# Optimization experiments

Measured on AMD Instinct MI355X. Metric: run time of the kernel, lower is better.

Reference implementation:

```python
import jax, jax.numpy as jnp
import numpy as np

NEG_SLOPE = 0.2


def gat_layer(x, W, a_src, a_dst, b, src, dst, num_nodes, heads, out_c, concat):
    # Linear transform per head: [N, heads, out_c]
    h = (x @ W).reshape(num_nodes, heads, out_c)
    # Per-node attention logits for source/dest roles: [N, heads]
    e_src = jnp.einsum('nhc,hc->nh', h, a_src)
    e_dst = jnp.einsum('nhc,hc->nh', h, a_dst)
    # Edge-wise scores (gather), LeakyReLU: [E, heads]
    e = jax.nn.leaky_relu(e_src[src] + e_dst[dst], negative_slope=NEG_SLOPE)
    # Segment softmax over incoming edges of each destination node
    m = jax.ops.segment_max(e, dst, num_segments=num_nodes)
    ex = jnp.exp(e - m[dst])
    denom = jax.ops.segment_sum(ex, dst, num_segments=num_nodes)
    alpha = ex / denom[dst]                       # [E, heads]
    # Weighted scatter-aggregate of source messages: [N, heads, out_c]
    out = jax.ops.segment_sum(h[src] * alpha[:, :, None], dst, num_segments=num_nodes)
    if concat:
        out = out.reshape(num_nodes, heads * out_c)
    else:
        out = out.mean(axis=1)
    return out + b


def setup_inputs() -> dict:
    key = jax.random.key(0)
    ks = jax.random.split(key, 12)
    N, E = 50000, 800000
    in_c, out_c, heads = 128, 32, 4
    x = jax.random.normal(ks[0], (N, in_c), dtype=jnp.float32)
    edge_index = jax.random.randint(ks[1], (2, E), 0, N, dtype=jnp.int64)
    s1 = 1.0 / np.sqrt(in_c)
    W1 = jax.random.normal(ks[2], (in_c, heads * out_c), dtype=jnp.float32) * s1
    a_src1 = jax.random.normal(ks[3], (heads, out_c), dtype=jnp.float32) * 0.1
    a_dst1 = jax.random.normal(ks[4], (heads, out_c), dtype=jnp.float32) * 0.1
    b1 = jnp.zeros((heads * out_c,), dtype=jnp.float32)
    s2 = 1.0 / np.sqrt(heads * out_c)
    W2 = jax.random.normal(ks[5], (heads * out_c, out_c), dtype=jnp.float32) * s2
    a_src2 = jax.random.normal(ks[6], (1, out_c), dtype=jnp.float32) * 0.1
    a_dst2 = jax.random.normal(ks[7], (1, out_c), dtype=jnp.float32) * 0.1
    b2 = jnp.zeros((out_c,), dtype=jnp.float32)
    return {"x": x, "edge_index": edge_index, "W1": W1, "a_src1": a_src1,
            "a_dst1": a_dst1, "b1": b1, "W2": W2, "a_src2": a_src2,
            "a_dst2": a_dst2, "b2": b2}


def reference(x, edge_index, W1, a_src1, a_dst1, b1, W2, a_src2, a_dst2, b2):
    N = x.shape[0]
    heads, out_c = a_src1.shape
    # add_self_loops=True (PyG default)
    loops = jnp.arange(N, dtype=edge_index.dtype)
    src = jnp.concatenate([edge_index[0], loops])
    dst = jnp.concatenate([edge_index[1], loops])
    h1 = gat_layer(x, W1, a_src1, a_dst1, b1, src, dst, N, heads, out_c, concat=True)
    h1 = jax.nn.elu(h1)
    out = gat_layer(h1, W2, a_src2, a_dst2, b2, src, dst, N, 1, out_c, concat=False)
    return out
```

## Files before the change

### kernel.cpp

```cpp
#include <hip/hip_runtime.h>
#include <hip/hip_bf16.h>

#define LRELU_SLOPE 0.2f
#define NB_SHIFT 7
#define NBLK 512

typedef __attribute__((ext_vector_type(8))) short short8;
typedef __attribute__((ext_vector_type(4))) float float4v;

__device__ inline float b2f(unsigned short u) {
    union { unsigned int i; float f; } v; v.i = ((unsigned int)u) << 16; return v.f;
}
__device__ inline unsigned short f2b(float f) {
    union { float f; unsigned int i; } v; v.f = f;
    unsigned int x = v.i;
    unsigned int r = x + 0x7fffu + ((x >> 16) & 1u);
    return (unsigned short)(r >> 16);
}
__device__ inline float lrelu(float x) { return x > 0.f ? x : LRELU_SLOPE * x; }

__global__ __launch_bounds__(256) void gemm1_mfma_kernel(
        const float* __restrict__ x, const float* __restrict__ W1,
        const float* __restrict__ a_src, const float* __restrict__ a_dst,
        unsigned short* __restrict__ h1b, float* __restrict__ es,
        float* __restrict__ ed, int N,
        const int* __restrict__ dst, int E, int Etot, int nb, int chunk,
        int* __restrict__ cnt) {
    __shared__ unsigned short xs[64][136];
    __shared__ unsigned short wt[128][136];
    int tid = threadIdx.x;
    int n0 = blockIdx.x * 64;

    for (int i = tid; i < 128 * 128; i += 256) {
        int k = i >> 7, n = i & 127;
        wt[n][k] = f2b(W1[i]);
    }
    {
        int rows = N - n0; if (rows > 64) rows = 64;
        const float4* xv = (const float4*)(x + (size_t)n0 * 128);
        int lim = rows * 32;
        for (int i = tid; i < lim; i += 256) {
            float4 v = xv[i];
            int r = i >> 5, c4 = (i & 31) << 2;
            uint2 p;
            p.x = (unsigned int)f2b(v.x) | ((unsigned int)f2b(v.y) << 16);
            p.y = (unsigned int)f2b(v.z) | ((unsigned int)f2b(v.w) << 16);
            *(uint2*)&xs[r][c4] = p;
        }
    }
    __syncthreads();

    int wave = tid >> 6;
    int lane = tid & 63;
    int lrow = lane & 15;
    int quad = lane >> 4;

    short8 afr[4];
#pragma unroll
    for (int kc = 0; kc < 4; kc++)
        afr[kc] = *(const short8*)&xs[wave * 16 + lrow][kc * 32 + quad * 8];
    __syncthreads();

#pragma unroll
    for (int ct = 0; ct < 8; ct++) {
        float4v acc = {0.f, 0.f, 0.f, 0.f};
#pragma unroll
        for (int kc = 0; kc < 4; kc++) {
            short8 bfr = *(const short8*)&wt[ct * 16 + lrow][kc * 32 + quad * 8];
            acc = __builtin_amdgcn_mfma_f32_16x16x32_bf16(afr[kc], bfr, acc, 0, 0, 0);
        }
#pragma unroll
        for (int r = 0; r < 4; r++) {
            int lr = wave * 16 + quad * 4 + r;
            int grow = n0 + lr;
            unsigned short hb = f2b(acc[r]);
            xs[lr][ct * 16 + lrow] = hb;
            if (grow < N)
                h1b[grow * 128 + ct * 16 + lrow] = hb;
        }
    }
    __syncthreads();

    int row = tid >> 2, h = tid & 3;
    int rg = n0 + row;
    if (rg < N) {
        const float* ap = a_src + h * 32;
        const float* bp = a_dst + h * 32;
        float s = 0.f, d = 0.f;
#pragma unroll
        for (int c2 = 0; c2 < 16; c2++) {
            unsigned int u = *(const unsigned int*)&xs[row][h * 32 + 2 * c2];
            float v0 = b2f((unsigned short)(u & 0xffffu));
            float v1 = b2f((unsigned short)(u >> 16));
            float2 a = *(const float2*)&ap[2 * c2];
            float2 b = *(const float2*)&bp[2 * c2];
            s += v0 * a.x + v1 * a.y;
            d += v0 * b.x + v1 * b.y;
        }
        es[rg * 4 + h] = s;
        ed[rg * 4 + h] = d;
    }

    int* histm = (int*)&wt[0][0];
    int blk = blockIdx.x;
    if (blk < NBLK)
        for (int i = tid; i < nb; i += 256) histm[i] = 0;
    __syncthreads();
    if (blk < NBLK) {
        int lo = blk * chunk;
        int hi = lo + chunk; if (hi > Etot) hi = Etot;
        for (int i = lo + tid; i < hi; i += 256) {
            int d = (i < E) ? dst[i] : (i - E);
            atomicAdd(&histm[d >> NB_SHIFT], 1);
        }
    }
    __syncthreads();
    if (blk < NBLK)
        for (int b = tid; b < nb; b += 256)
            cnt[b * NBLK + blk] = histm[b];
}

__global__ __launch_bounds__(1024) void scanA_kernel(int* cnt, int* bsum, int M) {
    __shared__ int tile[1024];
    int i = blockIdx.x * 1024 + threadIdx.x;
    int v = (i < M) ? cnt[i] : 0;
    tile[threadIdx.x] = v;
    __syncthreads();
    for (int off = 1; off < 1024; off <<= 1) {
        int t = (threadIdx.x >= (unsigned)off) ? tile[threadIdx.x - off] : 0;
        __syncthreads();
        tile[threadIdx.x] += t;
        __syncthreads();
    }
    int incl = tile[threadIdx.x];
    if (i < M) cnt[i] = incl - v;
    if (threadIdx.x == 1023) bsum[blockIdx.x] = incl;
}

__device__ inline void boff_scan(const int* __restrict__ bsum, int nbA,
                                 int* boffl, int tid) {
    int v = (tid < nbA) ? bsum[tid] : 0;
    boffl[tid] = v;
    __syncthreads();
    for (int off = 1; off < 256; off <<= 1) {
        int t = (tid >= off) ? boffl[tid - off] : 0;
        __syncthreads();
        boffl[tid] += t;
        __syncthreads();
    }
    int excl = boffl[tid] - v;
    __syncthreads();
    boffl[tid] = excl;
    __syncthreads();
}

__global__ __launch_bounds__(256) void partition_kernel(
        const int* __restrict__ src, const int* __restrict__ dst,
        int E, int Etot, int nb, int chunk, int nbA,
        const int* __restrict__ cnt, const int* __restrict__ bsum,
        unsigned int* __restrict__ bkt) {
    __shared__ int cur[512];
    __shared__ int boffl[256];
    int tid = threadIdx.x;
    boff_scan(bsum, nbA, boffl, tid);
    int blk = blockIdx.x;
    for (int b = tid; b < nb; b += 256) {
        int idx = b * NBLK + blk;
        cur[b] = cnt[idx] + boffl[idx >> 10];
    }
    __syncthreads();
    int lo = blk * chunk;
    int hi = lo + chunk; if (hi > Etot) hi = Etot;
    for (int i = lo + tid; i < hi; i += 256) {
        int s, d;
        if (i < E) { s = src[i]; d = dst[i]; }
        else       { s = d = i - E; }
        int pos = atomicAdd(&cur[d >> NB_SHIFT], 1);
        bkt[pos] = ((unsigned int)(d & 127) << 20) | (unsigned int)s;
    }
}

__global__ __launch_bounds__(256) void finalize_kernel(
        const unsigned int* __restrict__ bkt, const int* __restrict__ cnt,
        const int* __restrict__ bsum, int nb, int nbA,
        const float* __restrict__ es, const float* __restrict__ ed,
        int* __restrict__ ptr, int* __restrict__ csr_src,
        _Float16* __restrict__ w1h, int N, int Etot) {
    __shared__ int deg[128];
    __shared__ int scn[128];
    __shared__ int cur[128];
    __shared__ int boffl[256];
    int tid = threadIdx.x;
    boff_scan(bsum, nbA, boffl, tid);
    int b = blockIdx.x;
    int idx0 = b * NBLK;
    int base = cnt[idx0] + boffl[idx0 >> 10];
    int nextbase;
    if (b + 1 < nb) {
        int idx1 = (b + 1) * NBLK;
        nextbase = cnt[idx1] + boffl[idx1 >> 10];
    } else nextbase = Etot;
    int count = nextbase - base;
    int node0 = b << NB_SHIFT;
    int nodes = N - node0; if (nodes > 128) nodes = 128;

    if (tid < 128) deg[tid] = 0;
    __syncthreads();
    for (int i = tid; i < count; i += 256)
        atomicAdd(&deg[bkt[base + i] >> 20], 1);
    __syncthreads();
    int v = (tid < 128) ? deg[tid] : 0;
    if (tid < 128) scn[tid] = v;
    __syncthreads();
    for (int off = 1; off < 128; off <<= 1) {
        int t = (tid < 128 && tid >= (unsigned)off) ? scn[tid - off] : 0;
        __syncthreads();
        if (tid < 128) scn[tid] += t;
        __syncthreads();
    }
    if (tid < 128) {
        int excl = scn[tid] - v;
        cur[tid] = excl;
        if (tid < nodes) ptr[node0 + tid] = base + excl;
    }
    if (b == nb - 1 && tid == 0) ptr[N] = Etot;
    __syncthreads();
    for (int i = tid; i < count; i += 256) {
        unsigned int p = bkt[base + i];
        int dloc = p >> 20;
        int s = (int)(p & 0xFFFFFu);
        int pos = base + atomicAdd(&cur[dloc], 1);
        csr_src[pos] = s;
        float4 a = *(const float4*)&es[s * 4];
        float4 bb = *(const float4*)&ed[(node0 + dloc) * 4];
        union { _Float16 h[4]; uint2 u; } ww;
        ww.h[0] = (_Float16)__expf(lrelu(a.x + bb.x));
        ww.h[1] = (_Float16)__expf(lrelu(a.y + bb.y));
        ww.h[2] = (_Float16)__expf(lrelu(a.z + bb.z));
        ww.h[3] = (_Float16)__expf(lrelu(a.w + bb.w));
        *(uint2*)&w1h[(size_t)pos * 4] = ww.u;
    }
}

__global__ __launch_bounds__(256) void gemm2_mfma_kernel(
        const unsigned short* __restrict__ h1e, const float* __restrict__ W2,
        const float* __restrict__ a_src, const float* __restrict__ a_dst,
        unsigned short* __restrict__ h2b, float* __restrict__ es,
        float* __restrict__ ed, int N) {
    __shared__ unsigned short xs[64][136];
    __shared__ unsigned short wt[32][136];
    int tid = threadIdx.x;
    int n0 = blockIdx.x * 64;

    for (int i = tid; i < 128 * 32; i += 256) {
        int k = i >> 5, n = i & 31;
        wt[n][k] = f2b(W2[i]);
    }
    {
        const unsigned int* srcp = (const unsigned int*)(h1e + (size_t)n0 * 128);
        int rows = (N - n0) < 64 ? (N - n0) : 64;
        int maxu = rows * 64;
        for (int i = tid; i < 4096; i += 256) {
            unsigned int v = (i < maxu) ? srcp[i] : 0u;
            int r = i >> 6, cp = (i & 63) << 1;
            *(unsigned int*)&xs[r][cp] = v;
        }
    }
    __syncthreads();

    int wave = tid >> 6;
    int lane = tid & 63;
    int lrow = lane & 15;
    int quad = lane >> 4;

    short8 afr[4];
#pragma unroll
    for (int kc = 0; kc < 4; kc++)
        afr[kc] = *(const short8*)&xs[wave * 16 + lrow][kc * 32 + quad * 8];
    __syncthreads();

#pragma unroll
    for (int ct = 0; ct < 2; ct++) {
        float4v acc = {0.f, 0.f, 0.f, 0.f};
#pragma unroll
        for (int kc = 0; kc < 4; kc++) {
            short8 bfr = *(const short8*)&wt[ct * 16 + lrow][kc * 32 + quad * 8];
            acc = __builtin_amdgcn_mfma_f32_16x16x32_bf16(afr[kc], bfr, acc, 0, 0, 0);
        }
#pragma unroll
        for (int r = 0; r < 4; r++) {
            int lr = wave * 16 + quad * 4 + r;
            int grow = n0 + lr;
            unsigned short hb = f2b(acc[r]);
            xs[lr][ct * 16 + lrow] = hb;
            if (grow < N)
                h2b[(size_t)grow * 32 + ct * 16 + lrow] = hb;
        }
    }
    __syncthreads();

    if (tid < 64) {
        int rg = n0 + tid;
        if (rg < N) {
            float s = 0.f, d = 0.f;
#pragma unroll
            for (int c2 = 0; c2 < 16; c2++) {
                unsigned int u = *(const unsigned int*)&xs[tid][2 * c2];
                float v0 = b2f((unsigned short)(u & 0xffffu));
                float v1 = b2f((unsigned short)(u >> 16));
                float2 a = *(const float2*)&a_src[2 * c2];
                float2 b = *(const float2*)&a_dst[2 * c2];
                s += v0 * a.x + v1 * a.y;
                d += v0 * b.x + v1 * b.y;
            }
            es[rg] = s;
            ed[rg] = d;
        }
    }
}

__global__ __launch_bounds__(256) void agg1_kernel(
        const uint4* __restrict__ h1v, const _Float16* __restrict__ w1h,
        const int* __restrict__ csr, const int* __restrict__ ptr,
        const float* __restrict__ b1, uint4* __restrict__ h1e_v, int N) {
    int tid = threadIdx.x;
    int n = blockIdx.x * 16 + (tid >> 4);
    if (n >= N) return;
    int cl = tid & 15;
    int h = cl >> 2;
    int start = ptr[n], end = ptr[n + 1];
    float a0 = 0.f, a1 = 0.f, a2 = 0.f, a3 = 0.f;
    float a4 = 0.f, a5 = 0.f, a6 = 0.f, a7 = 0.f, ws = 0.f;
    int i = start;
    for (; i + 4 <= end; i += 4) {
        int s[4]; float v[4]; uint4 g[4];
#pragma unroll
        for (int k = 0; k < 4; k++) s[k] = csr[i + k];
#pragma unroll
        for (int k = 0; k < 4; k++) v[k] = (float)w1h[(size_t)(i + k) * 4 + h];
#pragma unroll
        for (int k = 0; k < 4; k++) g[k] = h1v[(s[k] << 4) + cl];
#pragma unroll
        for (int k = 0; k < 4; k++) {
            a0 += v[k] * b2f((unsigned short)(g[k].x & 0xffffu));
            a1 += v[k] * b2f((unsigned short)(g[k].x >> 16));
            a2 += v[k] * b2f((unsigned short)(g[k].y & 0xffffu));
            a3 += v[k] * b2f((unsigned short)(g[k].y >> 16));
            a4 += v[k] * b2f((unsigned short)(g[k].z & 0xffffu));
            a5 += v[k] * b2f((unsigned short)(g[k].z >> 16));
            a6 += v[k] * b2f((unsigned short)(g[k].w & 0xffffu));
            a7 += v[k] * b2f((unsigned short)(g[k].w >> 16));
            ws += v[k];
        }
    }
    for (; i < end; i++) {
        int s = csr[i];
        float v = (float)w1h[(size_t)i * 4 + h];
        uint4 g = h1v[(s << 4) + cl];
        a0 += v * b2f((unsigned short)(g.x & 0xffffu));
        a1 += v * b2f((unsigned short)(g.x >> 16));
        a2 += v * b2f((unsigned short)(g.y & 0xffffu));
        a3 += v * b2f((unsigned short)(g.y >> 16));
        a4 += v * b2f((unsigned short)(g.z & 0xffffu));
        a5 += v * b2f((unsigned short)(g.z >> 16));
        a6 += v * b2f((unsigned short)(g.w & 0xffffu));
        a7 += v * b2f((unsigned short)(g.w >> 16));
        ws += v;
    }
    float r = 1.f / ws;
    float4 bb0 = ((const float4*)b1)[cl * 2];
    float4 bb1 = ((const float4*)b1)[cl * 2 + 1];
    float o0 = a0 * r + bb0.x;
    float o1 = a1 * r + bb0.y;
    float o2 = a2 * r + bb0.z;
    float o3 = a3 * r + bb0.w;
    float o4 = a4 * r + bb1.x;
    float o5 = a5 * r + bb1.y;
    float o6 = a6 * r + bb1.z;
    float o7 = a7 * r + bb1.w;
    o0 = o0 > 0.f ? o0 : __expf(o0) - 1.f;
    o1 = o1 > 0.f ? o1 : __expf(o1) - 1.f;
    o2 = o2 > 0.f ? o2 : __expf(o2) - 1.f;
    o3 = o3 > 0.f ? o3 : __expf(o3) - 1.f;
    o4 = o4 > 0.f ? o4 : __expf(o4) - 1.f;
    o5 = o5 > 0.f ? o5 : __expf(o5) - 1.f;
    o6 = o6 > 0.f ? o6 : __expf(o6) - 1.f;
    o7 = o7 > 0.f ? o7 : __expf(o7) - 1.f;
    uint4 outv;
    outv.x = (unsigned int)f2b(o0) | ((unsigned int)f2b(o1) << 16);
    outv.y = (unsigned int)f2b(o2) | ((unsigned int)f2b(o3) << 16);
    outv.z = (unsigned int)f2b(o4) | ((unsigned int)f2b(o5) << 16);
    outv.w = (unsigned int)f2b(o6) | ((unsigned int)f2b(o7) << 16);
    h1e_v[(n << 4) + cl] = outv;
}

__global__ __launch_bounds__(256) void agg2_kernel(
        const uint2* __restrict__ h2v, const float* __restrict__ es,
        const float* __restrict__ ed, const int* __restrict__ csr,
        const int* __restrict__ ptr, const float* __restrict__ b2,
        float* __restrict__ out, int N) {
    int tid = threadIdx.x;
    int n = blockIdx.x * 32 + (tid >> 3);
    if (n >= N) return;
    int cl = tid & 7;
    float edl = ed[n];
    int start = ptr[n], end = ptr[n + 1];
    float a0 = 0.f, a1 = 0.f, a2 = 0.f, a3 = 0.f, ws = 0.f;
    int i = start;
    for (; i + 8 <= end; i += 8) {
        int s[8]; float e[8]; uint2 g[8];
#pragma unroll
        for (int k = 0; k < 8; k++) s[k] = csr[i + k];
#pragma unroll
        for (int k = 0; k < 8; k++) e[k] = es[s[k]];
#pragma unroll
        for (int k = 0; k < 8; k++) g[k] = h2v[(s[k] << 3) + cl];
#pragma unroll
        for (int k = 0; k < 8; k++) {
            float v = __expf(lrelu(e[k] + edl));
            a0 += v * b2f((unsigned short)(g[k].x & 0xffffu));
            a1 += v * b2f((unsigned short)(g[k].x >> 16));
            a2 += v * b2f((unsigned short)(g[k].y & 0xffffu));
            a3 += v * b2f((unsigned short)(g[k].y >> 16));
            ws += v;
        }
    }
    for (; i < end; i++) {
        int s = csr[i];
        float v = __expf(lrelu(es[s] + edl));
        uint2 g = h2v[(s << 3) + cl];
        a0 += v * b2f((unsigned short)(g.x & 0xffffu));
        a1 += v * b2f((unsigned short)(g.x >> 16));
        a2 += v * b2f((unsigned short)(g.y & 0xffffu));
        a3 += v * b2f((unsigned short)(g.y >> 16));
        ws += v;
    }
    float r = 1.f / ws;
    float4 bb = ((const float4*)b2)[cl];
    float4 o;
    o.x = a0 * r + bb.x;
    o.y = a1 * r + bb.y;
    o.z = a2 * r + bb.z;
    o.w = a3 * r + bb.w;
    ((float4*)out)[(size_t)n * 8 + cl] = o;
}

extern "C" void kernel_launch(void* const* d_in, const int* in_sizes, int n_in,
                              void* d_out, int out_size, void* d_ws, size_t ws_size,
                              hipStream_t stream) {
    const float* x      = (const float*)d_in[0];
    const int*   ei     = (const int*)  d_in[1];
    const float* W1     = (const float*)d_in[2];
    const float* a_src1 = (const float*)d_in[3];
    const float* a_dst1 = (const float*)d_in[4];
    const float* b1     = (const float*)d_in[5];
    const float* W2     = (const float*)d_in[6];
    const float* a_src2 = (const float*)d_in[7];
    const float* a_dst2 = (const float*)d_in[8];
    const float* b2     = (const float*)d_in[9];
    float* outp = (float*)d_out;

    const int N = in_sizes[0] / 128;
    const int E = in_sizes[1] / 2;
    const int Etot = E + N;

    const int* src = ei;
    const int* dst = ei + E;

    const int nb    = (N + 127) >> 7;
    const int chunk = (Etot + NBLK - 1) / NBLK;
    const int M = nb * NBLK;
    const int nbA = (M + 1023) / 1024;

    char* w = (char*)d_ws;
    unsigned short* h1b = (unsigned short*)(w + 0);
    unsigned short* h1e = (unsigned short*)(w + 12800000);
    unsigned short* h2b = (unsigned short*)(w + 25600000);
    float* es1  = (float*)(w + 28800000);
    float* ed1  = (float*)(w + 29600000);
    float* es2  = (float*)(w + 30400000);
    float* ed2  = (float*)(w + 30600000);
    int*   ptr  = (int*)  (w + 30800000);
    int*   bsum = (int*)  (w + 31000064);
    int*   cnt  = (int*)  (w + 31001088);
    int*   csr_src = (int*)(w + 31801856);
    unsigned int* bkt = (unsigned int*)(w + 35201856);
    _Float16* w1h = (_Float16*)(w + 42001856);

    gemm1_mfma_kernel<<<(N + 63) / 64, 256, 0, stream>>>(x, W1, a_src1, a_dst1,
                                                         h1b, es1, ed1, N,
                                                         dst, E, Etot, nb, chunk,
                                                         cnt);

    scanA_kernel<<<nbA, 1024, 0, stream>>>(cnt, bsum, M);
    partition_kernel<<<NBLK, 256, 0, stream>>>(src, dst, E, Etot, nb, chunk, nbA,
                                               cnt, bsum, bkt);
    finalize_kernel<<<nb, 256, 0, stream>>>(bkt, cnt, bsum, nb, nbA, es1, ed1,
                                            ptr, csr_src, w1h, N, Etot);

    agg1_kernel<<<(N + 15) / 16, 256, 0, stream>>>((const uint4*)h1b, w1h,
                                                   csr_src, ptr, b1,
                                                   (uint4*)h1e, N);

    gemm2_mfma_kernel<<<(N + 63) / 64, 256, 0, stream>>>(h1e, W2, a_src2, a_dst2,
                                                         h2b, es2, ed2, N);
    agg2_kernel<<<(N + 31) / 32, 256, 0, stream>>>((const uint2*)h2b, es2, ed2,
                                                   csr_src, ptr, b2, outp, N);
}
```

Baseline: 198.7 us.

## Replace bucketed two-pass CSR build with global-atomic degree count and direct placement

The CSR construction moves from a bucket histogram, partition and per-bucket finalize scheme to per-node global atomic degree counting, a single exclusive scan over N, and one placement pass that writes each edge directly using global atomics. This removes the intermediate bucket buffer and one full pass over the edges. In exchange it adds heavy contention on global atomics, since each of the ~850k edges does an atomicAdd on a per-node counter. W1 and W2 are also converted to bf16 and transposed once in a new prep kernel, so each GEMM block loads them with vector copies instead of converting them itself. CSR order within a node becomes nondeterministic.

```diff
diff --git a/kernel.cpp b/kernel.cpp
--- a/kernel.cpp
+++ b/kernel.cpp
@@ -2,8 +2,6 @@
 #include <hip/hip_bf16.h>
 
 #define LRELU_SLOPE 0.2f
-#define NB_SHIFT 7
-#define NBLK 512
 
 typedef __attribute__((ext_vector_type(8))) short short8;
 typedef __attribute__((ext_vector_type(4))) float float4v;
@@ -19,21 +17,41 @@
 }
 __device__ inline float lrelu(float x) { return x > 0.f ? x : LRELU_SLOPE * x; }
 
+__global__ __launch_bounds__(256) void prep_kernel(
+        const float* __restrict__ W1, const float* __restrict__ W2,
+        unsigned short* __restrict__ w1t, unsigned short* __restrict__ w2t,
+        int* __restrict__ deg, int N) {
+    int gid = blockIdx.x * 256 + threadIdx.x;
+    int gstride = gridDim.x * 256;
+    for (int i = gid; i < N; i += gstride) deg[i] = 0;
+    for (int i = gid; i < 16384; i += gstride) {
+        int n = i >> 7, k = i & 127;
+        w1t[i] = f2b(W1[k * 128 + n]);
+    }
+    for (int i = gid; i < 4096; i += gstride) {
+        int n = i >> 7, k = i & 127;
+        w2t[i] = f2b(W2[k * 32 + n]);
+    }
+}
+
 __global__ __launch_bounds__(256) void gemm1_mfma_kernel(
-        const float* __restrict__ x, const float* __restrict__ W1,
+        const float* __restrict__ x, const unsigned short* __restrict__ w1t,
         const float* __restrict__ a_src, const float* __restrict__ a_dst,
         unsigned short* __restrict__ h1b, float* __restrict__ es,
         float* __restrict__ ed, int N,
-        const int* __restrict__ dst, int E, int Etot, int nb, int chunk,
-        int* __restrict__ cnt) {
+        const int* __restrict__ dst, int E, int Etot,
+        int* __restrict__ deg) {
     __shared__ unsigned short xs[64][136];
     __shared__ unsigned short wt[128][136];
     int tid = threadIdx.x;
     int n0 = blockIdx.x * 64;
 
-    for (int i = tid; i < 128 * 128; i += 256) {
-        int k = i >> 7, n = i & 127;
-        wt[n][k] = f2b(W1[i]);
+    {
+        const uint4* wv = (const uint4*)w1t;
+        for (int i = tid; i < 2048; i += 256) {
+            int n = i >> 4, k8 = i & 15;
+            *(uint4*)&wt[n][k8 * 8] = wv[i];
+        }
     }
     {
         int rows = N - n0; if (rows > 64) rows = 64;
@@ -101,29 +119,20 @@
         ed[rg * 4 + h] = d;
     }
 
-    int* histm = (int*)&wt[0][0];
-    int blk = blockIdx.x;
-    if (blk < NBLK)
-        for (int i = tid; i < nb; i += 256) histm[i] = 0;
-    __syncthreads();
-    if (blk < NBLK) {
-        int lo = blk * chunk;
-        int hi = lo + chunk; if (hi > Etot) hi = Etot;
-        for (int i = lo + tid; i < hi; i += 256) {
-            int d = (i < E) ? dst[i] : (i - E);
-            atomicAdd(&histm[d >> NB_SHIFT], 1);
-        }
-    }
-    __syncthreads();
-    if (blk < NBLK)
-        for (int b = tid; b < nb; b += 256)
-            cnt[b * NBLK + blk] = histm[b];
-}
-
-__global__ __launch_bounds__(1024) void scanA_kernel(int* cnt, int* bsum, int M) {
+    int gid = blockIdx.x * 256 + tid;
+    int gstride = gridDim.x * 256;
+    for (int i = gid; i < Etot; i += gstride) {
+        int d = (i < E) ? dst[i] : (i - E);
+        atomicAdd(&deg[d], 1);
+    }
+}
+
+__global__ __launch_bounds__(1024) void scanP1_kernel(
+        int* __restrict__ cur, int* __restrict__ loc,
+        int* __restrict__ psum, int M) {
     __shared__ int tile[1024];
     int i = blockIdx.x * 1024 + threadIdx.x;
-    int v = (i < M) ? cnt[i] : 0;
+    int v = (i < M) ? cur[i] : 0;
     tile[threadIdx.x] = v;
     __syncthreads();
     for (int off = 1; off < 1024; off <<= 1) {
@@ -133,13 +142,14 @@
         __syncthreads();
     }
     int incl = tile[threadIdx.x];
-    if (i < M) cnt[i] = incl - v;
-    if (threadIdx.x == 1023) bsum[blockIdx.x] = incl;
-}
-
-__device__ inline void boff_scan(const int* __restrict__ bsum, int nbA,
+    int excl = incl - v;
+    if (i < M) { cur[i] = excl; loc[i] = excl; }
+    if (threadIdx.x == 1023) psum[blockIdx.x] = incl;
+}
+
+__device__ inline void boff_scan(const int* __restrict__ psum, int nt,
                                  int* boffl, int tid) {
-    int v = (tid < nbA) ? bsum[tid] : 0;
+    int v = (tid < nt) ? psum[tid] : 0;
     boffl[tid] = v;
     __syncthreads();
     for (int off = 1; off < 256; off <<= 1) {
@@ -154,85 +164,28 @@
     __syncthreads();
 }
 
-__global__ __launch_bounds__(256) void partition_kernel(
+__global__ __launch_bounds__(256) void place_kernel(
         const int* __restrict__ src, const int* __restrict__ dst,
-        int E, int Etot, int nb, int chunk, int nbA,
-        const int* __restrict__ cnt, const int* __restrict__ bsum,
-        unsigned int* __restrict__ bkt) {
-    __shared__ int cur[512];
+        int E, int Etot, int N,
+        const int* __restrict__ loc, const int* __restrict__ psum, int nt,
+        int* __restrict__ cur,
+        const float* __restrict__ es, const float* __restrict__ ed,
+        int* __restrict__ ptr, int* __restrict__ csr_src,
+        _Float16* __restrict__ w1h) {
     __shared__ int boffl[256];
     int tid = threadIdx.x;
-    boff_scan(bsum, nbA, boffl, tid);
-    int blk = blockIdx.x;
-    for (int b = tid; b < nb; b += 256) {
-        int idx = b * NBLK + blk;
-        cur[b] = cnt[idx] + boffl[idx >> 10];
-    }
-    __syncthreads();
-    int lo = blk * chunk;
-    int hi = lo + chunk; if (hi > Etot) hi = Etot;
-    for (int i = lo + tid; i < hi; i += 256) {
+    boff_scan(psum, nt, boffl, tid);
+    int gid = blockIdx.x * 256 + tid;
+    if (gid <= N)
+        ptr[gid] = (gid < N) ? (loc[gid] + boffl[gid >> 10]) : Etot;
+    if (gid < Etot) {
         int s, d;
-        if (i < E) { s = src[i]; d = dst[i]; }
-        else       { s = d = i - E; }
-        int pos = atomicAdd(&cur[d >> NB_SHIFT], 1);
-        bkt[pos] = ((unsigned int)(d & 127) << 20) | (unsigned int)s;
-    }
-}
-
-__global__ __launch_bounds__(256) void finalize_kernel(
-        const unsigned int* __restrict__ bkt, const int* __restrict__ cnt,
-        const int* __restrict__ bsum, int nb, int nbA,
-        const float* __restrict__ es, const float* __restrict__ ed,
-        int* __restrict__ ptr, int* __restrict__ csr_src,
-        _Float16* __restrict__ w1h, int N, int Etot) {
-    __shared__ int deg[128];
-    __shared__ int scn[128];
-    __shared__ int cur[128];
-    __shared__ int boffl[256];
-    int tid = threadIdx.x;
-    boff_scan(bsum, nbA, boffl, tid);
-    int b = blockIdx.x;
-    int idx0 = b * NBLK;
-    int base = cnt[idx0] + boffl[idx0 >> 10];
-    int nextbase;
-    if (b + 1 < nb) {
-        int idx1 = (b + 1) * NBLK;
-        nextbase = cnt[idx1] + boffl[idx1 >> 10];
-    } else nextbase = Etot;
-    int count = nextbase - base;
-    int node0 = b << NB_SHIFT;
-    int nodes = N - node0; if (nodes > 128) nodes = 128;
-
-    if (tid < 128) deg[tid] = 0;
-    __syncthreads();
-    for (int i = tid; i < count; i += 256)
-        atomicAdd(&deg[bkt[base + i] >> 20], 1);
-    __syncthreads();
-    int v = (tid < 128) ? deg[tid] : 0;
-    if (tid < 128) scn[tid] = v;
-    __syncthreads();
-    for (int off = 1; off < 128; off <<= 1) {
-        int t = (tid < 128 && tid >= (unsigned)off) ? scn[tid - off] : 0;
-        __syncthreads();
-        if (tid < 128) scn[tid] += t;
-        __syncthreads();
-    }
-    if (tid < 128) {
-        int excl = scn[tid] - v;
-        cur[tid] = excl;
-        if (tid < nodes) ptr[node0 + tid] = base + excl;
-    }
-    if (b == nb - 1 && tid == 0) ptr[N] = Etot;
-    __syncthreads();
-    for (int i = tid; i < count; i += 256) {
-        unsigned int p = bkt[base + i];
-        int dloc = p >> 20;
-        int s = (int)(p & 0xFFFFFu);
-        int pos = base + atomicAdd(&cur[dloc], 1);
+        if (gid < E) { s = src[gid]; d = dst[gid]; }
+        else         { s = d = gid - E; }
+        int pos = boffl[d >> 10] + atomicAdd(&cur[d], 1);
         csr_src[pos] = s;
         float4 a = *(const float4*)&es[s * 4];
-        float4 bb = *(const float4*)&ed[(node0 + dloc) * 4];
+        float4 bb = *(const float4*)&ed[d * 4];
         union { _Float16 h[4]; uint2 u; } ww;
         ww.h[0] = (_Float16)__expf(lrelu(a.x + bb.x));
         ww.h[1] = (_Float16)__expf(lrelu(a.y + bb.y));
@@ -243,7 +196,7 @@
 }
 
 __global__ __launch_bounds__(256) void gemm2_mfma_kernel(
-        const unsigned short* __restrict__ h1e, const float* __restrict__ W2,
+        const unsigned short* __restrict__ h1e, const unsigned short* __restrict__ w2t,
         const float* __restrict__ a_src, const float* __restrict__ a_dst,
         unsigned short* __restrict__ h2b, float* __restrict__ es,
         float* __restrict__ ed, int N) {
@@ -252,9 +205,12 @@
     int tid = threadIdx.x;
     int n0 = blockIdx.x * 64;
 
-    for (int i = tid; i < 128 * 32; i += 256) {
-        int k = i >> 5, n = i & 31;
-        wt[n][k] = f2b(W2[i]);
+    {
+        const uint4* wv = (const uint4*)w2t;
+        for (int i = tid; i < 512; i += 256) {
+            int n = i >> 4, k8 = i & 15;
+            *(uint4*)&wt[n][k8 * 8] = wv[i];
+        }
     }
     {
         const unsigned int* srcp = (const unsigned int*)(h1e + (size_t)n0 * 128);
@@ -467,10 +423,7 @@
     const int* src = ei;
     const int* dst = ei + E;
 
-    const int nb    = (N + 127) >> 7;
-    const int chunk = (Etot + NBLK - 1) / NBLK;
-    const int M = nb * NBLK;
-    const int nbA = (M + 1023) / 1024;
+    const int ntile = (N + 1023) / 1024;
 
     char* w = (char*)d_ws;
     unsigned short* h1b = (unsigned short*)(w + 0);
@@ -481,28 +434,31 @@
     float* es2  = (float*)(w + 30400000);
     float* ed2  = (float*)(w + 30600000);
     int*   ptr  = (int*)  (w + 30800000);
-    int*   bsum = (int*)  (w + 31000064);
-    int*   cnt  = (int*)  (w + 31001088);
+    int*   psum = (int*)  (w + 31000064);
+    int*   deg  = (int*)  (w + 31001088);
+    int*   loc  = (int*)  (w + 31201280);
     int*   csr_src = (int*)(w + 31801856);
-    unsigned int* bkt = (unsigned int*)(w + 35201856);
+    unsigned short* w1t = (unsigned short*)(w + 35201856);
+    unsigned short* w2t = (unsigned short*)(w + 35234624);
     _Float16* w1h = (_Float16*)(w + 42001856);
 
-    gemm1_mfma_kernel<<<(N + 63) / 64, 256, 0, stream>>>(x, W1, a_src1, a_dst1,
+    prep_kernel<<<64, 256, 0, stream>>>(W1, W2, w1t, w2t, deg, N);
+
+    gemm1_mfma_kernel<<<(N + 63) / 64, 256, 0, stream>>>(x, w1t, a_src1, a_dst1,
                                                          h1b, es1, ed1, N,
-                                                         dst, E, Etot, nb, chunk,
-                                                         cnt);
-
-    scanA_kernel<<<nbA, 1024, 0, stream>>>(cnt, bsum, M);
-    partition_kernel<<<NBLK, 256, 0, stream>>>(src, dst, E, Etot, nb, chunk, nbA,
-                                               cnt, bsum, bkt);
-    finalize_kernel<<<nb, 256, 0, stream>>>(bkt, cnt, bsum, nb, nbA, es1, ed1,
-                                            ptr, csr_src, w1h, N, Etot);
+                                                         dst, E, Etot, deg);
+
+    scanP1_kernel<<<ntile, 1024, 0, stream>>>(deg, loc, psum, N);
+    place_kernel<<<(Etot + 255) / 256, 256, 0, stream>>>(src, dst, E, Etot, N,
+                                                         loc, psum, ntile, deg,
+                                                         es1, ed1, ptr, csr_src,
+                                                         w1h);
 
     agg1_kernel<<<(N + 15) / 16, 256, 0, stream>>>((const uint4*)h1b, w1h,
                                                    csr_src, ptr, b1,
                                                    (uint4*)h1e, N);
 
-    gemm2_mfma_kernel<<<(N + 63) / 64, 256, 0, stream>>>(h1e, W2, a_src2, a_dst2,
+    gemm2_mfma_kernel<<<(N + 63) / 64, 256, 0, stream>>>(h1e, w2t, a_src2, a_dst2,
                                                          h2b, es2, ed2, N);
     agg2_kernel<<<(N + 31) / 32, 256, 0, stream>>>((const uint2*)h2b, es2, ed2,
                                                    csr_src, ptr, b2, outp, N);
```

Result: slower. 248.1 us (+24.9%).
